# Kernel optimization log

Measured on AMD Instinct MI355X. Metric: run time of the kernel, lower is better.

Reference implementation:

```python
import jax, jax.numpy as jnp
from jax import lax
import numpy as np


def _gru_cell(x, h, wih, whh, bih, bhh):
    # torch.nn.GRUCell math: gates split order (r, z, n)
    gi = x @ wih.T + bih          # (N, 3H)
    gh = h @ whh.T + bhh          # (N, 3H)
    ir, iz, i_n = jnp.split(gi, 3, axis=-1)
    hr, hz, h_n = jnp.split(gh, 3, axis=-1)
    r = jax.nn.sigmoid(ir + hr)
    z = jax.nn.sigmoid(iz + hz)
    n = jnp.tanh(i_n + r * h_n)
    return (1.0 - z) * n + z * h


def _dilated_gru(x, dilation, wih, whh, bih, bhh):
    # h_i depends on h_{i-dilation} -> `dilation` independent chains,
    # scanned jointly with a carried state of shape (B*dilation, H).
    B, S, I = x.shape
    H = whh.shape[1]
    nc = S // dilation  # assumes S % dilation == 0
    xr = x.reshape(B, nc, dilation, I).transpose(1, 0, 2, 3).reshape(nc, B * dilation, I)

    def step(h, xt):
        hn = _gru_cell(xt, h, wih, whh, bih, bhh)
        return hn, hn

    h0 = jnp.zeros((B * dilation, H), x.dtype)
    _, ys = lax.scan(step, h0, xr)  # (nc, B*dilation, H)
    return ys.reshape(nc, B, dilation, H).transpose(1, 0, 2, 3).reshape(B, S, H)


def _encoder(data, fparams, bparams, dilations):
    outs = []
    x = data
    for p, d in zip(fparams, dilations):
        x = _dilated_gru(x, d, *p)
        outs.append(x[:, -1, :])
    x = data[:, ::-1, :]
    for p, d in zip(bparams, dilations):
        x = _dilated_gru(x, d, *p)
        outs.append(x[:, -1, :])
    return jnp.concatenate(outs, axis=1)  # (B, 2*sum(hidden_sizes)) = (B, 400)


def setup_inputs() -> dict:
    key = jax.random.key(0)
    ks = jax.random.split(key, 7)
    B, S = 1024, 512
    sizes = [(1, 100), (100, 50), (50, 50)]  # (input_size, hidden_size) per layer

    def cell(k, iS, H):
        k1, k2, k3, k4 = jax.random.split(k, 4)
        s = 1.0 / np.sqrt(H)  # torch GRUCell init: U(-1/sqrt(H), 1/sqrt(H))
        u = lambda kk, shp: jax.random.uniform(kk, shp, jnp.float32, -s, s)
        return u(k1, (3 * H, iS)), u(k2, (3 * H, H)), u(k3, (3 * H,)), u(k4, (3 * H,))

    d = {"data": jax.random.normal(ks[0], (B, S, 1), jnp.float32)}
    for i, nm in enumerate(["f1", "f2", "f3", "b1", "b2", "b3"]):
        iS, H = sizes[i % 3]
        w1, w2, bb1, bb2 = cell(ks[i + 1], iS, H)
        d[nm + "_wih"] = w1
        d[nm + "_whh"] = w2
        d[nm + "_bih"] = bb1
        d[nm + "_bhh"] = bb2
    return d


def reference(data,
              f1_wih, f1_whh, f1_bih, f1_bhh,
              f2_wih, f2_whh, f2_bih, f2_bhh,
              f3_wih, f3_whh, f3_bih, f3_bhh,
              b1_wih, b1_whh, b1_bih, b1_bhh,
              b2_wih, b2_whh, b2_bih, b2_bhh,
              b3_wih, b3_whh, b3_bih, b3_bhh):
    dilations = (1, 4, 16)
    fparams = [(f1_wih, f1_whh, f1_bih, f1_bhh),
               (f2_wih, f2_whh, f2_bih, f2_bhh),
               (f3_wih, f3_whh, f3_bih, f3_bhh)]
    bparams = [(b1_wih, b1_whh, b1_bih, b1_bhh),
               (b2_wih, b2_whh, b2_bih, b2_bhh),
               (b3_wih, b3_whh, b3_bih, b3_bhh)]
    return _encoder(data, fparams, bparams, dilations)
```

## Files before the change

kernel.cpp:

```cpp
#include <hip/hip_runtime.h>
#include <math.h>

typedef short  s16x8 __attribute__((ext_vector_type(8)));
typedef float  f32x4 __attribute__((ext_vector_type(4)));

static __device__ __forceinline__ float sigf(float x){ return 1.0f/(1.0f+__expf(-x)); }
static __device__ __forceinline__ float tanhf_fast(float x){
  float ax=fabsf(x); float e=__expf(-2.0f*ax); float t=(1.0f-e)/(1.0f+e); return copysignf(t,x);
}
static __device__ __forceinline__ unsigned short f2bf(float x){
  unsigned int u = __float_as_uint(x);
  unsigned int r = (u + 0x7FFFu + ((u >> 16) & 1u)) >> 16;
  return (unsigned short)r;
}
static __device__ __forceinline__ float bf2f(unsigned short b){
  return __uint_as_float(((unsigned int)b) << 16);
}
static __device__ __forceinline__ unsigned int cvt_pk_bf16(float a, float b){
  unsigned int r;
  asm("v_cvt_pk_bf16_f32 %0, %1, %2" : "=v"(r) : "v"(a), "v"(b));
  return r;
}
static __device__ __forceinline__ void fast_barrier(){
  asm volatile("s_waitcnt lgkmcnt(0)" ::: "memory");
  __builtin_amdgcn_s_barrier();
}
static __device__ __forceinline__ float qsum(float v){
  v += __int_as_float(__builtin_amdgcn_mov_dpp(__float_as_int(v),0xB1,0xF,0xF,true));
  v += __int_as_float(__builtin_amdgcn_mov_dpp(__float_as_int(v),0x4E,0xF,0xF,true));
  return v;
}
static __device__ __forceinline__ float rsum4(float v){
  return v + __int_as_float(__builtin_amdgcn_ds_swizzle(__float_as_int(v), 0x101F));
}
static __device__ __forceinline__ float sel4(int c, float4 v){
  float r=v.x; r=(c==1)?v.y:r; r=(c==2)?v.z:r; r=(c==3)?v.w:r; return r;
}

static __device__ __forceinline__ void load_afrag(const float* __restrict__ whh,
                                                  int gate, int tile, int l, int kc,
                                                  s16x8& hi, s16x8& lo){
  const int r  = tile*16 + (l & 15);
  const int kb = kc*32 + (l >> 4)*8;
  #pragma unroll
  for (int j = 0; j < 8; ++j){
    const int k = kb + j;
    const float wv = (r < 100 && k < 100) ? whh[(size_t)(gate*100 + r)*100 + k] : 0.0f;
    const unsigned short hb = f2bf(wv);
    hi[j] = (short)hb;
    lo[j] = (short)f2bf(wv - bf2f(hb));
  }
}

__global__ __launch_bounds__(448, 2)
void gru_l1(const float* __restrict__ data,
            const float* __restrict__ wih_f, const float* __restrict__ whh_f,
            const float* __restrict__ bih_f, const float* __restrict__ bhh_f,
            const float* __restrict__ wih_b, const float* __restrict__ whh_b,
            const float* __restrict__ bih_b, const float* __restrict__ bhh_b,
            float* __restrict__ x1f, float* __restrict__ x1b,
            float* __restrict__ out)
{
  const int dir   = (int)(blockIdx.x >> 6);
  const int blk16 = (int)(blockIdx.x & 63);
  const int t     = (int)threadIdx.x;
  const float* __restrict__ wih = dir ? wih_b : wih_f;
  const float* __restrict__ whh = dir ? whh_b : whh_f;
  const float* __restrict__ bih = dir ? bih_b : bih_f;
  const float* __restrict__ bhh = dir ? bhh_b : bhh_f;
  float* __restrict__ x1 = dir ? x1b : x1f;
  const int obase = dir ? 200 : 0;
  const int b0 = blk16 * 16;

  __shared__ __align__(16) unsigned short hBhi[2][16][136];
  __shared__ __align__(16) unsigned short hBlo[2][16][136];
  __shared__ __align__(16) float xs[512][16];

  for (int i = t; i < 8192; i += 448){
    const int c  = i >> 9;
    const int sL = i & 511;
    xs[sL][c] = data[(size_t)(b0 + c)*512 + (size_t)(dir ? (511 - sL) : sL)];
  }
  { unsigned short* ph = (unsigned short*)hBhi;
    unsigned short* pl = (unsigned short*)hBlo;
    for (int i = t; i < 2*16*136; i += 448){ ph[i] = 0; pl[i] = 0; } }

  const int l  = t & 63;
  const int W  = t >> 6;

  s16x8 AH00,AH01,AH02,AH03, AH10,AH11,AH12,AH13, AH20,AH21,AH22,AH23;
  s16x8 AL00,AL01,AL02,AL03, AL10,AL11,AL12,AL13, AL20,AL21,AL22,AL23;
  #define LDA(G,KC) load_afrag(whh, G, W, l, KC, AH##G##KC, AL##G##KC);
  LDA(0,0) LDA(0,1) LDA(0,2) LDA(0,3)
  LDA(1,0) LDA(1,1) LDA(1,2) LDA(1,3)
  LDA(2,0) LDA(2,1) LDA(2,2) LDA(2,3)
  #undef LDA

  const int mg  = (l >> 4) * 4;
  const int u0  = W*16 + mg;
  const bool uvalid = (u0 < 100);
  const int u0c = uvalid ? u0 : 96;
  const int c   = l & 15;
  const f32x4 wxr4 = *(const f32x4*)&wih[u0c];
  const f32x4 wxz4 = *(const f32x4*)&wih[100 + u0c];
  const f32x4 wxn4 = *(const f32x4*)&wih[200 + u0c];
  const f32x4 bcr4 = *(const f32x4*)&bih[u0c]       + *(const f32x4*)&bhh[u0c];
  const f32x4 bcz4 = *(const f32x4*)&bih[100 + u0c] + *(const f32x4*)&bhh[100 + u0c];
  const f32x4 bxn4 = *(const f32x4*)&bih[200 + u0c];
  const f32x4 bhn4 = *(const f32x4*)&bhh[200 + u0c];
  f32x4 hprev = {0.f,0.f,0.f,0.f};

  __syncthreads();

  const int bn = c;
  const int bg = (l >> 4)*8;

  #pragma unroll 1
  for (int s = 0; s < 512; ++s){
    const int cur = s & 1, nxt = cur ^ 1;

    const s16x8 BH0 = *(const s16x8*)&hBhi[cur][bn][ 0 + bg];
    const s16x8 BL0 = *(const s16x8*)&hBlo[cur][bn][ 0 + bg];
    const s16x8 BH1 = *(const s16x8*)&hBhi[cur][bn][32 + bg];
    const s16x8 BL1 = *(const s16x8*)&hBlo[cur][bn][32 + bg];
    const s16x8 BH2 = *(const s16x8*)&hBhi[cur][bn][64 + bg];
    const s16x8 BL2 = *(const s16x8*)&hBlo[cur][bn][64 + bg];
    const s16x8 BH3 = *(const s16x8*)&hBhi[cur][bn][96 + bg];
    const s16x8 BL3 = *(const s16x8*)&hBlo[cur][bn][96 + bg];

    f32x4 Ca0={0.f,0.f,0.f,0.f}, Cb0={0.f,0.f,0.f,0.f};
    f32x4 Ca1={0.f,0.f,0.f,0.f}, Cb1={0.f,0.f,0.f,0.f};
    f32x4 Ca2={0.f,0.f,0.f,0.f}, Cb2={0.f,0.f,0.f,0.f};
    #define MM(ACC,G,KC) \
      ACC = __builtin_amdgcn_mfma_f32_16x16x32_bf16(AL##G##KC, BH##KC, ACC, 0, 0, 0); \
      ACC = __builtin_amdgcn_mfma_f32_16x16x32_bf16(AH##G##KC, BL##KC, ACC, 0, 0, 0); \
      ACC = __builtin_amdgcn_mfma_f32_16x16x32_bf16(AH##G##KC, BH##KC, ACC, 0, 0, 0);
    MM(Ca0,0,0) MM(Ca1,1,0) MM(Ca2,2,0)
    MM(Cb0,0,2) MM(Cb1,1,2) MM(Cb2,2,2)
    MM(Ca0,0,1) MM(Ca1,1,1) MM(Ca2,2,1)
    MM(Cb0,0,3) MM(Cb1,1,3) MM(Cb2,2,3)
    #undef MM
    const f32x4 sr = Ca0 + Cb0;
    const f32x4 sz = Ca1 + Cb1;
    const f32x4 sn = Ca2 + Cb2;

    const float xc = xs[s][c];
    f32x4 hn;
    #define FIN(I) { \
      const float rr = sigf(sr[I] + fmaf(wxr4[I], xc, bcr4[I])); \
      const float zz = sigf(sz[I] + fmaf(wxz4[I], xc, bcz4[I])); \
      const float nn = tanhf_fast(fmaf(wxn4[I], xc, bxn4[I]) + rr*(sn[I] + bhn4[I])); \
      hn[I] = nn + zz*(hprev[I] - nn); }
    FIN(0) FIN(1) FIN(2) FIN(3)
    #undef FIN
    hprev = hn;

    if (uvalid){
      const unsigned int px = cvt_pk_bf16(hn[0], hn[1]);
      const unsigned int py = cvt_pk_bf16(hn[2], hn[3]);
      const float l0 = hn[0] - __uint_as_float(px << 16);
      const float l1 = hn[1] - __uint_as_float(px & 0xFFFF0000u);
      const float l2 = hn[2] - __uint_as_float(py << 16);
      const float l3 = hn[3] - __uint_as_float(py & 0xFFFF0000u);
      uint2 vhi; vhi.x = px; vhi.y = py;
      uint2 vlo; vlo.x = cvt_pk_bf16(l0, l1); vlo.y = cvt_pk_bf16(l2, l3);
      *(uint2*)&hBhi[nxt][c][u0] = vhi;
      *(uint2*)&hBlo[nxt][c][u0] = vlo;
      if ((s & 3) == 3){
        const int cs = s >> 2;
        const int ch = b0 + c;
        *(f32x4*)&x1[((size_t)cs*1024 + ch)*100 + u0] = hn;
      }
      if (s == 511){
        const int ch = b0 + c;
        *(f32x4*)&out[(size_t)ch*400 + obase + u0] = hn;
      }
    }
    fast_barrier();
  }
}

static __device__ __forceinline__ float l2w(const float* __restrict__ wih,
                                            const float* __restrict__ whh,
                                            int sec, int r, int k){
  if (r >= 50) return 0.f;
  if (sec == 2) return (k < 100) ? wih[(size_t)(100 + r)*100 + k] : 0.f;
  if (sec == 3) return (k >= 104 && k < 154) ? whh[(size_t)(100 + r)*50 + (k - 104)] : 0.f;
  const int ro = (sec == 1) ? 50 : 0;
  if (k < 100) return wih[(size_t)(ro + r)*100 + k];
  if (k >= 104 && k < 154) return whh[(size_t)(ro + r)*50 + (k - 104)];
  return 0.f;
}
static __device__ __forceinline__ void l2_afrag(const float* __restrict__ wih,
                                                const float* __restrict__ whh,
                                                int sec, int tile, int l, int kc,
                                                s16x8& hi, s16x8& lo){
  const int r  = tile*16 + (l & 15);
  const int kb = kc*32 + (l >> 4)*8;
  #pragma unroll
  for (int j = 0; j < 8; ++j){
    const float wv = l2w(wih, whh, sec, r, kb + j);
    const unsigned short hb = f2bf(wv);
    hi[j] = (short)hb;
    lo[j] = (short)f2bf(wv - bf2f(hb));
  }
}

__global__ __launch_bounds__(256, 1)
void gru_l2(const float* __restrict__ x1f, const float* __restrict__ x1b,
            const float* __restrict__ wih_f, const float* __restrict__ whh_f,
            const float* __restrict__ bih_f, const float* __restrict__ bhh_f,
            const float* __restrict__ wih_b, const float* __restrict__ whh_b,
            const float* __restrict__ bih_b, const float* __restrict__ bhh_b,
            float* __restrict__ x2f, float* __restrict__ x2b,
            float* __restrict__ out)
{
  const int dir   = (int)(blockIdx.x >> 6);
  const int blk16 = (int)(blockIdx.x & 63);
  const int t     = (int)threadIdx.x;
  const float* __restrict__ wih = dir ? wih_b : wih_f;
  const float* __restrict__ whh = dir ? whh_b : whh_f;
  const float* __restrict__ bih = dir ? bih_b : bih_f;
  const float* __restrict__ bhh = dir ? bhh_b : bhh_f;
  const float* __restrict__ x1 = dir ? x1b : x1f;
  float* __restrict__ x2 = dir ? x2b : x2f;
  const int obase = dir ? 300 : 100;
  const int b0 = blk16 * 16;

  __shared__ __align__(16) unsigned short hBhi[2][16][168];
  __shared__ __align__(16) unsigned short hBlo[2][16][168];

  { unsigned short* ph = (unsigned short*)hBhi;
    unsigned short* pl = (unsigned short*)hBlo;
    for (int i = t; i < 2*16*168; i += 256){ ph[i] = 0; pl[i] = 0; } }

  const int l = t & 63;
  const int W = t >> 6;

  s16x8 AH00,AH01,AH02,AH03,AH04, AH10,AH11,AH12,AH13,AH14,
        AH20,AH21,AH22,AH23,AH24, AH30,AH31,AH32,AH33,AH34;
  s16x8 AL00,AL01,AL02,AL03,AL04, AL10,AL11,AL12,AL13,AL14,
        AL20,AL21,AL22,AL23,AL24, AL30,AL31,AL32,AL33,AL34;
  #define LDA(SE,KC) l2_afrag(wih, whh, SE, W, l, KC, AH##SE##KC, AL##SE##KC);
  LDA(0,0) LDA(0,1) LDA(0,2) LDA(0,3) LDA(0,4)
  LDA(1,0) LDA(1,1) LDA(1,2) LDA(1,3) LDA(1,4)
  LDA(2,0) LDA(2,1) LDA(2,2) LDA(2,3) LDA(2,4)
  LDA(3,0) LDA(3,1) LDA(3,2) LDA(3,3) LDA(3,4)
  #undef LDA

  const int mg = (l >> 4) * 4;
  const int c  = l & 15;
  const int u0 = W*16 + mg;
  const int ch = b0 + c;
  f32x4 bcr, bcz, bxn, bhn;
  #pragma unroll
  for (int i = 0; i < 4; ++i){
    const int u = (u0 + i < 50) ? (u0 + i) : 49;
    bcr[i] = bih[u]      + bhh[u];
    bcz[i] = bih[50 + u] + bhh[50 + u];
    bxn[i] = bih[100 + u];
    bhn[i] = bhh[100 + u];
  }
  const bool vH = (u0 < 50);
  f32x4 hp = {0.f,0.f,0.f,0.f};

  float* px = x2 + (((size_t)(ch >> 2))*50 + u0)*4 + (ch & 3);
  const size_t X2STRIDE = (size_t)256*50*4;

  const int oct  = t >> 4;
  const int cc   = t & 15;
  const bool stg = (t < 208);
  const int u0x  = oct * 8;

  __syncthreads();

  if (stg){
    const float* p = x1 + ((size_t)0*1024 + (b0 + cc))*100;
    f32x4 va = *(const f32x4*)&p[u0x];
    f32x4 vb = {0.f,0.f,0.f,0.f};
    if (u0x + 4 < 100) vb = *(const f32x4*)&p[u0x + 4];
    unsigned int h0 = cvt_pk_bf16(va[0], va[1]);
    unsigned int h1 = cvt_pk_bf16(va[2], va[3]);
    unsigned int h2 = cvt_pk_bf16(vb[0], vb[1]);
    unsigned int h3 = cvt_pk_bf16(vb[2], vb[3]);
    uint4 vhi; vhi.x=h0; vhi.y=h1; vhi.z=h2; vhi.w=h3;
    uint4 vlo;
    vlo.x = cvt_pk_bf16(va[0]-__uint_as_float(h0<<16), va[1]-__uint_as_float(h0&0xFFFF0000u));
    vlo.y = cvt_pk_bf16(va[2]-__uint_as_float(h1<<16), va[3]-__uint_as_float(h1&0xFFFF0000u));
    vlo.z = cvt_pk_bf16(vb[0]-__uint_as_float(h2<<16), vb[1]-__uint_as_float(h2&0xFFFF0000u));
    vlo.w = cvt_pk_bf16(vb[2]-__uint_as_float(h3<<16), vb[3]-__uint_as_float(h3&0xFFFF0000u));
    *(uint4*)&hBhi[0][cc][u0x] = vhi;
    *(uint4*)&hBlo[0][cc][u0x] = vlo;
  }
  __syncthreads();

  const int bn = c;
  const int bg = (l >> 4)*8;

  #pragma unroll 1
  for (int s = 0; s < 128; ++s){
    const int cur = s & 1, nxt = cur ^ 1;

    f32x4 va = {0.f,0.f,0.f,0.f}, vb = {0.f,0.f,0.f,0.f};
    if (stg){
      const int st = (s + 1 < 128) ? (s + 1) : 127;
      const float* p = x1 + ((size_t)st*1024 + (b0 + cc))*100;
      va = *(const f32x4*)&p[u0x];
      if (u0x + 4 < 100) vb = *(const f32x4*)&p[u0x + 4];
    }

    const s16x8 BH0 = *(const s16x8*)&hBhi[cur][bn][  0 + bg];
    const s16x8 BL0 = *(const s16x8*)&hBlo[cur][bn][  0 + bg];
    const s16x8 BH1 = *(const s16x8*)&hBhi[cur][bn][ 32 + bg];
    const s16x8 BL1 = *(const s16x8*)&hBlo[cur][bn][ 32 + bg];
    const s16x8 BH2 = *(const s16x8*)&hBhi[cur][bn][ 64 + bg];
    const s16x8 BL2 = *(const s16x8*)&hBlo[cur][bn][ 64 + bg];
    const s16x8 BH3 = *(const s16x8*)&hBhi[cur][bn][ 96 + bg];
    const s16x8 BL3 = *(const s16x8*)&hBlo[cur][bn][ 96 + bg];
    const s16x8 BH4 = *(const s16x8*)&hBhi[cur][bn][128 + bg];
    const s16x8 BL4 = *(const s16x8*)&hBlo[cur][bn][128 + bg];

    f32x4 CrA={0.f,0.f,0.f,0.f}, CzA={0.f,0.f,0.f,0.f}, CxA={0.f,0.f,0.f,0.f}, ChA={0.f,0.f,0.f,0.f};
    f32x4 CrB={0.f,0.f,0.f,0.f}, CzB={0.f,0.f,0.f,0.f}, CxB={0.f,0.f,0.f,0.f}, ChB={0.f,0.f,0.f,0.f};
    #define MF(ACC,A,B) ACC = __builtin_amdgcn_mfma_f32_16x16x32_bf16(A, B, ACC, 0, 0, 0);
    #define G4(SET,KC,AOP,BOP) \
      MF(Cr##SET, AOP##0##KC, BOP##KC) MF(Cz##SET, AOP##1##KC, BOP##KC) \
      MF(Cx##SET, AOP##2##KC, BOP##KC) MF(Ch##SET, AOP##3##KC, BOP##KC)
    G4(A,0,AL,BH) G4(B,3,AL,BH) G4(A,1,AL,BH) G4(B,4,AL,BH) G4(A,2,AL,BH)
    G4(A,0,AH,BL) G4(B,3,AH,BL) G4(A,1,AH,BL) G4(B,4,AH,BL) G4(A,2,AH,BL)
    G4(A,0,AH,BH) G4(B,3,AH,BH) G4(A,1,AH,BH) G4(B,4,AH,BH) G4(A,2,AH,BH)
    #undef G4
    #undef MF
    const f32x4 Cr = CrA + CrB;
    const f32x4 Cz = CzA + CzB;
    const f32x4 Cx = CxA + CxB;
    const f32x4 Ch = ChA + ChB;

    f32x4 hn;
    #define FIN(I) { \
      const float rr = sigf(Cr[I] + bcr[I]); \
      const float zz = sigf(Cz[I] + bcz[I]); \
      const float nn = tanhf_fast(Cx[I] + bxn[I] + rr*(Ch[I] + bhn[I])); \
      hn[I] = nn + zz*(hp[I] - nn); }
    FIN(0) FIN(1) FIN(2) FIN(3)
    #undef FIN
    hp = hn;

    if (vH){
      const unsigned int p0 = cvt_pk_bf16(hn[0], hn[1]);
      const unsigned int p1 = cvt_pk_bf16(hn[2], hn[3]);
      const float l0 = hn[0] - __uint_as_float(p0 << 16);
      const float l1 = hn[1] - __uint_as_float(p0 & 0xFFFF0000u);
      const float l2 = hn[2] - __uint_as_float(p1 << 16);
      const float l3 = hn[3] - __uint_as_float(p1 & 0xFFFF0000u);
      uint2 whi; whi.x = p0; whi.y = p1;
      uint2 wlo; wlo.x = cvt_pk_bf16(l0, l1); wlo.y = cvt_pk_bf16(l2, l3);
      *(uint2*)&hBhi[nxt][c][104 + u0] = whi;
      *(uint2*)&hBlo[nxt][c][104 + u0] = wlo;
      if ((s & 3) == 3){
        if (u0 + 0 < 50) px[ 0] = hn[0];
        if (u0 + 1 < 50) px[ 4] = hn[1];
        if (u0 + 2 < 50) px[ 8] = hn[2];
        if (u0 + 3 < 50) px[12] = hn[3];
        px += X2STRIDE;
      }
      if (s == 127){
        if (u0 + 0 < 50) out[(size_t)ch*400 + obase + u0 + 0] = hn[0];
        if (u0 + 1 < 50) out[(size_t)ch*400 + obase + u0 + 1] = hn[1];
        if (u0 + 2 < 50) out[(size_t)ch*400 + obase + u0 + 2] = hn[2];
        if (u0 + 3 < 50) out[(size_t)ch*400 + obase + u0 + 3] = hn[3];
      }
    }

    if (stg){
      unsigned int h0 = cvt_pk_bf16(va[0], va[1]);
      unsigned int h1 = cvt_pk_bf16(va[2], va[3]);
      unsigned int h2 = cvt_pk_bf16(vb[0], vb[1]);
      unsigned int h3 = cvt_pk_bf16(vb[2], vb[3]);
      uint4 vhi; vhi.x=h0; vhi.y=h1; vhi.z=h2; vhi.w=h3;
      uint4 vlo;
      vlo.x = cvt_pk_bf16(va[0]-__uint_as_float(h0<<16), va[1]-__uint_as_float(h0&0xFFFF0000u));
      vlo.y = cvt_pk_bf16(va[2]-__uint_as_float(h1<<16), va[3]-__uint_as_float(h1&0xFFFF0000u));
      vlo.z = cvt_pk_bf16(vb[0]-__uint_as_float(h2<<16), vb[1]-__uint_as_float(h2&0xFFFF0000u));
      vlo.w = cvt_pk_bf16(vb[2]-__uint_as_float(h3<<16), vb[3]-__uint_as_float(h3&0xFFFF0000u));
      *(uint4*)&hBhi[nxt][cc][u0x] = vhi;
      *(uint4*)&hBlo[nxt][cc][u0x] = vlo;
    }
    fast_barrier();
  }
}

__global__ __launch_bounds__(512, 4)
void gru_l3(const float* __restrict__ x2f, const float* __restrict__ x2b,
            const float* __restrict__ wih_f, const float* __restrict__ whh_f,
            const float* __restrict__ bih_f, const float* __restrict__ bhh_f,
            const float* __restrict__ wih_b, const float* __restrict__ whh_b,
            const float* __restrict__ bih_b, const float* __restrict__ bhh_b,
            float* __restrict__ out)
{
  const int dir = (int)(blockIdx.x >> 8);
  const int blk = (int)(blockIdx.x & 255);
  const int t   = (int)threadIdx.x;
  const float* __restrict__ wih = dir ? wih_b : wih_f;
  const float* __restrict__ whh = dir ? whh_b : whh_f;
  const float* __restrict__ bih = dir ? bih_b : bih_f;
  const float* __restrict__ bhh = dir ? bhh_b : bhh_f;
  const float* __restrict__ x2 = dir ? x2b : x2f;
  const int obase = dir ? 350 : 150;
  const int b0 = blk * 4;

  __shared__ __align__(16) float xh[2][104][4];

  const int oct = t >> 3;
  const int u   = (oct > 49) ? 49 : oct;
  const int l   = t & 7;
  const int cb  = 13 * l;
  float4 W0,W1,W2,W3,W4,W5,W6,W7,W8,W9,W10,W11,W12;
  #define L3LW(J, V) { const int g = cb + (J); \
    const float wr_ = (g<50) ? wih[(size_t)(u     )*50+g] : ((g<100)? whh[(size_t)(u     )*50+g-50] : 0.f); \
    const float wz_ = (g<50) ? wih[(size_t)(u + 50)*50+g] : ((g<100)? whh[(size_t)(u + 50)*50+g-50] : 0.f); \
    const float wx_ = (g<50) ? wih[(size_t)(u +100)*50+g] : 0.f; \
    const float wh_ = (g>=50 && g<100) ? whh[(size_t)(u +100)*50+g-50] : 0.f; \
    V = make_float4(wr_, wz_, wx_, wh_); }
  L3LW(0,W0) L3LW(1,W1) L3LW(2,W2) L3LW(3,W3) L3LW(4,W4) L3LW(5,W5) L3LW(6,W6)
  L3LW(7,W7) L3LW(8,W8) L3LW(9,W9) L3LW(10,W10) L3LW(11,W11) L3LW(12,W12)
  #undef L3LW
  const float bcr = bih[u] + bhh[u];
  const float bcz = bih[u+50] + bhh[u+50];
  const float bxn = bih[u+100];
  const float bhn = bhh[u+100];

  for (int i = t; i < 108; i += 512){
    const int bi = (i >= 54) ? 1 : 0;
    const int row = 50 + (i - bi*54);
    *(float4*)&xh[bi][row][0] = make_float4(0.f,0.f,0.f,0.f);
  }
  if (t < 50)
    *(float4*)&xh[0][t][0] = *(const float4*)(x2 + (((size_t)0*256 + blk)*50 + t)*4);
  __syncthreads();

  #pragma unroll 1
  for (int s = 0; s < 32; ++s){
    const int cur = s & 1, nxt = cur ^ 1;
    if (t < 400){
      const float* hb = &xh[cur][cb][0];
      float ar0=0,ar1=0,ar2=0,ar3=0, az0=0,az1=0,az2=0,az3=0;
      float ax0=0,ax1=0,ax2=0,ax3=0, ah0=0,ah1=0,ah2=0,ah3=0;
      #define L3C(J, WV) { const float4 h4 = *(const float4*)(hb + 4*(J)); \
        ar0=fmaf(WV.x,h4.x,ar0); ar1=fmaf(WV.x,h4.y,ar1); ar2=fmaf(WV.x,h4.z,ar2); ar3=fmaf(WV.x,h4.w,ar3); \
        az0=fmaf(WV.y,h4.x,az0); az1=fmaf(WV.y,h4.y,az1); az2=fmaf(WV.y,h4.z,az2); az3=fmaf(WV.y,h4.w,az3); \
        ax0=fmaf(WV.z,h4.x,ax0); ax1=fmaf(WV.z,h4.y,ax1); ax2=fmaf(WV.z,h4.z,ax2); ax3=fmaf(WV.z,h4.w,ax3); \
        ah0=fmaf(WV.w,h4.x,ah0); ah1=fmaf(WV.w,h4.y,ah1); ah2=fmaf(WV.w,h4.z,ah2); ah3=fmaf(WV.w,h4.w,ah3); }
      L3C(0,W0) L3C(1,W1) L3C(2,W2) L3C(3,W3) L3C(4,W4) L3C(5,W5) L3C(6,W6)
      L3C(7,W7) L3C(8,W8) L3C(9,W9) L3C(10,W10) L3C(11,W11) L3C(12,W12)
      #undef L3C
      ar0=qsum(ar0); ar1=qsum(ar1); ar2=qsum(ar2); ar3=qsum(ar3);
      az0=qsum(az0); az1=qsum(az1); az2=qsum(az2); az3=qsum(az3);
      ax0=qsum(ax0); ax1=qsum(ax1); ax2=qsum(ax2); ax3=qsum(ax3);
      ah0=qsum(ah0); ah1=qsum(ah1); ah2=qsum(ah2); ah3=qsum(ah3);
      ar0=rsum4(ar0); ar1=rsum4(ar1); ar2=rsum4(ar2); ar3=rsum4(ar3);
      az0=rsum4(az0); az1=rsum4(az1); az2=rsum4(az2); az3=rsum4(az3);
      ax0=rsum4(ax0); ax1=rsum4(ax1); ax2=rsum4(ax2); ax3=rsum4(ax3);
      ah0=rsum4(ah0); ah1=rsum4(ah1); ah2=rsum4(ah2); ah3=rsum4(ah3);
      if (l < 4){
        const float Ar = sel4(l, make_float4(ar0,ar1,ar2,ar3));
        const float Az = sel4(l, make_float4(az0,az1,az2,az3));
        const float Ax = sel4(l, make_float4(ax0,ax1,ax2,ax3));
        const float Ah = sel4(l, make_float4(ah0,ah1,ah2,ah3));
        const float ho = xh[cur][50+u][l];
        const float r = sigf(Ar + bcr);
        const float z = sigf(Az + bcz);
        const float n = tanhf_fast(Ax + bxn + r*(Ah + bhn));
        const float hnew = n + z*(ho - n);
        xh[nxt][50+u][l] = hnew;
        if (s == 31) out[(size_t)(b0 + l)*400 + obase + u] = hnew;
      }
    } else if (t < 450){
      if (s + 1 < 32){
        const int j = t - 400;
        *(float4*)&xh[nxt][j][0] = *(const float4*)(x2 + (((size_t)(s+1)*256 + blk)*50 + j)*4);
      }
    }
    __syncthreads();
  }
}

extern "C" void kernel_launch(void* const* d_in, const int* in_sizes, int n_in,
                              void* d_out, int out_size, void* d_ws, size_t ws_size,
                              hipStream_t stream)
{
  const float* data   = (const float*)d_in[0];
  const float* f1_wih = (const float*)d_in[1];
  const float* f1_whh = (const float*)d_in[2];
  const float* f1_bih = (const float*)d_in[3];
  const float* f1_bhh = (const float*)d_in[4];
  const float* f2_wih = (const float*)d_in[5];
  const float* f2_whh = (const float*)d_in[6];
  const float* f2_bih = (const float*)d_in[7];
  const float* f2_bhh = (const float*)d_in[8];
  const float* f3_wih = (const float*)d_in[9];
  const float* f3_whh = (const float*)d_in[10];
  const float* f3_bih = (const float*)d_in[11];
  const float* f3_bhh = (const float*)d_in[12];
  const float* b1_wih = (const float*)d_in[13];
  const float* b1_whh = (const float*)d_in[14];
  const float* b1_bih = (const float*)d_in[15];
  const float* b1_bhh = (const float*)d_in[16];
  const float* b2_wih = (const float*)d_in[17];
  const float* b2_whh = (const float*)d_in[18];
  const float* b2_bih = (const float*)d_in[19];
  const float* b2_bhh = (const float*)d_in[20];
  const float* b3_wih = (const float*)d_in[21];
  const float* b3_whh = (const float*)d_in[22];
  const float* b3_bih = (const float*)d_in[23];
  const float* b3_bhh = (const float*)d_in[24];
  float* out = (float*)d_out;

  const size_t X1N = (size_t)128 * 1024 * 100;
  const size_t X2N = (size_t)32 * 256 * 50 * 4;
  if (ws_size < (2 * X1N + 2 * X2N) * sizeof(float)) return;
  float* wsf = (float*)d_ws;
  float* x1f = wsf;
  float* x1b = wsf + X1N;
  float* x2f = wsf + 2 * X1N;
  float* x2b = wsf + 2 * X1N + X2N;

  gru_l1<<<dim3(128), dim3(448), 0, stream>>>(
      data, f1_wih, f1_whh, f1_bih, f1_bhh,
      b1_wih, b1_whh, b1_bih, b1_bhh, x1f, x1b, out);
  gru_l2<<<dim3(128), dim3(256), 0, stream>>>(
      x1f, x1b, f2_wih, f2_whh, f2_bih, f2_bhh,
      b2_wih, b2_whh, b2_bih, b2_bhh, x2f, x2b, out);
  gru_l3<<<dim3(512), dim3(512), 0, stream>>>(
      x2f, x2b, f3_wih, f3_whh, f3_bih, f3_bhh,
      b3_wih, b3_whh, b3_bih, b3_bhh, out);
}
```

Before: 1.027 ms.

## Merge forward and backward directions into one block for layers 1 and 2

Layer 1 and layer 2 kernels now launch half as many blocks, each twice as large, with the forward and backward directions running as two thread groups in the same block and using separate shared-memory state. Layer 1 also drops the shared-memory staging of the input sequence and reads each scalar input straight from global memory every step. The per-step block barrier now synchronizes both directions together, so each direction waits on the slower one. The global input load sits on the critical path of every step, which may add latency to the sequential recurrence.

Result: slower. 3.346 ms (+226.0%).

```diff
diff --git a/kernel.cpp b/kernel.cpp
--- a/kernel.cpp
+++ b/kernel.cpp
@@ -52,7 +52,7 @@
   }
 }
 
-__global__ __launch_bounds__(448, 2)
+__global__ __launch_bounds__(896, 1)
 void gru_l1(const float* __restrict__ data,
             const float* __restrict__ wih_f, const float* __restrict__ whh_f,
             const float* __restrict__ bih_f, const float* __restrict__ bhh_f,
@@ -61,9 +61,11 @@
             float* __restrict__ x1f, float* __restrict__ x1b,
             float* __restrict__ out)
 {
-  const int dir   = (int)(blockIdx.x >> 6);
-  const int blk16 = (int)(blockIdx.x & 63);
+  const int blk16 = (int)blockIdx.x;
   const int t     = (int)threadIdx.x;
+  const int grp   = (t >= 448) ? 1 : 0;
+  const int tt    = t - grp*448;
+  const int dir   = grp;
   const float* __restrict__ wih = dir ? wih_b : wih_f;
   const float* __restrict__ whh = dir ? whh_b : whh_f;
   const float* __restrict__ bih = dir ? bih_b : bih_f;
@@ -72,21 +74,15 @@
   const int obase = dir ? 200 : 0;
   const int b0 = blk16 * 16;
 
-  __shared__ __align__(16) unsigned short hBhi[2][16][136];
-  __shared__ __align__(16) unsigned short hBlo[2][16][136];
-  __shared__ __align__(16) float xs[512][16];
-
-  for (int i = t; i < 8192; i += 448){
-    const int c  = i >> 9;
-    const int sL = i & 511;
-    xs[sL][c] = data[(size_t)(b0 + c)*512 + (size_t)(dir ? (511 - sL) : sL)];
-  }
-  { unsigned short* ph = (unsigned short*)hBhi;
-    unsigned short* pl = (unsigned short*)hBlo;
-    for (int i = t; i < 2*16*136; i += 448){ ph[i] = 0; pl[i] = 0; } }
-
-  const int l  = t & 63;
-  const int W  = t >> 6;
+  __shared__ __align__(16) unsigned short hBhi[2][2][16][136];
+  __shared__ __align__(16) unsigned short hBlo[2][2][16][136];
+
+  { unsigned short* ph = &hBhi[grp][0][0][0];
+    unsigned short* pl = &hBlo[grp][0][0][0];
+    for (int i = tt; i < 2*16*136; i += 448){ ph[i] = 0; pl[i] = 0; } }
+
+  const int l  = tt & 63;
+  const int W  = tt >> 6;
 
   s16x8 AH00,AH01,AH02,AH03, AH10,AH11,AH12,AH13, AH20,AH21,AH22,AH23;
   s16x8 AL00,AL01,AL02,AL03, AL10,AL11,AL12,AL13, AL20,AL21,AL22,AL23;
@@ -110,6 +106,8 @@
   const f32x4 bhn4 = *(const f32x4*)&bhh[200 + u0c];
   f32x4 hprev = {0.f,0.f,0.f,0.f};
 
+  const float* xptr = data + (size_t)(b0 + c)*512;
+
   __syncthreads();
 
   const int bn = c;
@@ -119,14 +117,16 @@
   for (int s = 0; s < 512; ++s){
     const int cur = s & 1, nxt = cur ^ 1;
 
-    const s16x8 BH0 = *(const s16x8*)&hBhi[cur][bn][ 0 + bg];
-    const s16x8 BL0 = *(const s16x8*)&hBlo[cur][bn][ 0 + bg];
-    const s16x8 BH1 = *(const s16x8*)&hBhi[cur][bn][32 + bg];
-    const s16x8 BL1 = *(const s16x8*)&hBlo[cur][bn][32 + bg];
-    const s16x8 BH2 = *(const s16x8*)&hBhi[cur][bn][64 + bg];
-    const s16x8 BL2 = *(const s16x8*)&hBlo[cur][bn][64 + bg];
-    const s16x8 BH3 = *(const s16x8*)&hBhi[cur][bn][96 + bg];
-    const s16x8 BL3 = *(const s16x8*)&hBlo[cur][bn][96 + bg];
+    const float xc = xptr[dir ? (511 - s) : s];
+
+    const s16x8 BH0 = *(const s16x8*)&hBhi[grp][cur][bn][ 0 + bg];
+    const s16x8 BL0 = *(const s16x8*)&hBlo[grp][cur][bn][ 0 + bg];
+    const s16x8 BH1 = *(const s16x8*)&hBhi[grp][cur][bn][32 + bg];
+    const s16x8 BL1 = *(const s16x8*)&hBlo[grp][cur][bn][32 + bg];
+    const s16x8 BH2 = *(const s16x8*)&hBhi[grp][cur][bn][64 + bg];
+    const s16x8 BL2 = *(const s16x8*)&hBlo[grp][cur][bn][64 + bg];
+    const s16x8 BH3 = *(const s16x8*)&hBhi[grp][cur][bn][96 + bg];
+    const s16x8 BL3 = *(const s16x8*)&hBlo[grp][cur][bn][96 + bg];
 
     f32x4 Ca0={0.f,0.f,0.f,0.f}, Cb0={0.f,0.f,0.f,0.f};
     f32x4 Ca1={0.f,0.f,0.f,0.f}, Cb1={0.f,0.f,0.f,0.f};
@@ -144,7 +144,6 @@
     const f32x4 sz = Ca1 + Cb1;
     const f32x4 sn = Ca2 + Cb2;
 
-    const float xc = xs[s][c];
     f32x4 hn;
     #define FIN(I) { \
       const float rr = sigf(sr[I] + fmaf(wxr4[I], xc, bcr4[I])); \
@@ -164,8 +163,8 @@
       const float l3 = hn[3] - __uint_as_float(py & 0xFFFF0000u);
       uint2 vhi; vhi.x = px; vhi.y = py;
       uint2 vlo; vlo.x = cvt_pk_bf16(l0, l1); vlo.y = cvt_pk_bf16(l2, l3);
-      *(uint2*)&hBhi[nxt][c][u0] = vhi;
-      *(uint2*)&hBlo[nxt][c][u0] = vlo;
+      *(uint2*)&hBhi[grp][nxt][c][u0] = vhi;
+      *(uint2*)&hBlo[grp][nxt][c][u0] = vlo;
       if ((s & 3) == 3){
         const int cs = s >> 2;
         const int ch = b0 + c;
@@ -206,7 +205,7 @@
   }
 }
 
-__global__ __launch_bounds__(256, 1)
+__global__ __launch_bounds__(512, 1)
 void gru_l2(const float* __restrict__ x1f, const float* __restrict__ x1b,
             const float* __restrict__ wih_f, const float* __restrict__ whh_f,
             const float* __restrict__ bih_f, const float* __restrict__ bhh_f,
@@ -215,9 +214,11 @@
             float* __restrict__ x2f, float* __restrict__ x2b,
             float* __restrict__ out)
 {
-  const int dir   = (int)(blockIdx.x >> 6);
-  const int blk16 = (int)(blockIdx.x & 63);
+  const int blk16 = (int)blockIdx.x;
   const int t     = (int)threadIdx.x;
+  const int grp   = (t >= 256) ? 1 : 0;
+  const int tt    = t - grp*256;
+  const int dir   = grp;
   const float* __restrict__ wih = dir ? wih_b : wih_f;
   const float* __restrict__ whh = dir ? whh_b : whh_f;
   const float* __restrict__ bih = dir ? bih_b : bih_f;
@@ -227,15 +228,15 @@
   const int obase = dir ? 300 : 100;
   const int b0 = blk16 * 16;
 
-  __shared__ __align__(16) unsigned short hBhi[2][16][168];
-  __shared__ __align__(16) unsigned short hBlo[2][16][168];
-
-  { unsigned short* ph = (unsigned short*)hBhi;
-    unsigned short* pl = (unsigned short*)hBlo;
-    for (int i = t; i < 2*16*168; i += 256){ ph[i] = 0; pl[i] = 0; } }
-
-  const int l = t & 63;
-  const int W = t >> 6;
+  __shared__ __align__(16) unsigned short hBhi[2][2][16][168];
+  __shared__ __align__(16) unsigned short hBlo[2][2][16][168];
+
+  { unsigned short* ph = &hBhi[grp][0][0][0];
+    unsigned short* pl = &hBlo[grp][0][0][0];
+    for (int i = tt; i < 2*16*168; i += 256){ ph[i] = 0; pl[i] = 0; } }
+
+  const int l = tt & 63;
+  const int W = tt >> 6;
 
   s16x8 AH00,AH01,AH02,AH03,AH04, AH10,AH11,AH12,AH13,AH14,
         AH20,AH21,AH22,AH23,AH24, AH30,AH31,AH32,AH33,AH34;
@@ -267,9 +268,9 @@
   float* px = x2 + (((size_t)(ch >> 2))*50 + u0)*4 + (ch & 3);
   const size_t X2STRIDE = (size_t)256*50*4;
 
-  const int oct  = t >> 4;
-  const int cc   = t & 15;
-  const bool stg = (t < 208);
+  const int oct  = tt >> 4;
+  const int cc   = tt & 15;
+  const bool stg = (tt < 208);
   const int u0x  = oct * 8;
 
   __syncthreads();
@@ -289,8 +290,8 @@
     vlo.y = cvt_pk_bf16(va[2]-__uint_as_float(h1<<16), va[3]-__uint_as_float(h1&0xFFFF0000u));
     vlo.z = cvt_pk_bf16(vb[0]-__uint_as_float(h2<<16), vb[1]-__uint_as_float(h2&0xFFFF0000u));
     vlo.w = cvt_pk_bf16(vb[2]-__uint_as_float(h3<<16), vb[3]-__uint_as_float(h3&0xFFFF0000u));
-    *(uint4*)&hBhi[0][cc][u0x] = vhi;
-    *(uint4*)&hBlo[0][cc][u0x] = vlo;
+    *(uint4*)&hBhi[grp][0][cc][u0x] = vhi;
+    *(uint4*)&hBlo[grp][0][cc][u0x] = vlo;
   }
   __syncthreads();
 
@@ -309,16 +310,16 @@
       if (u0x + 4 < 100) vb = *(const f32x4*)&p[u0x + 4];
     }
 
-    const s16x8 BH0 = *(const s16x8*)&hBhi[cur][bn][  0 + bg];
-    const s16x8 BL0 = *(const s16x8*)&hBlo[cur][bn][  0 + bg];
-    const s16x8 BH1 = *(const s16x8*)&hBhi[cur][bn][ 32 + bg];
-    const s16x8 BL1 = *(const s16x8*)&hBlo[cur][bn][ 32 + bg];
-    const s16x8 BH2 = *(const s16x8*)&hBhi[cur][bn][ 64 + bg];
-    const s16x8 BL2 = *(const s16x8*)&hBlo[cur][bn][ 64 + bg];
-    const s16x8 BH3 = *(const s16x8*)&hBhi[cur][bn][ 96 + bg];
-    const s16x8 BL3 = *(const s16x8*)&hBlo[cur][bn][ 96 + bg];
-    const s16x8 BH4 = *(const s16x8*)&hBhi[cur][bn][128 + bg];
-    const s16x8 BL4 = *(const s16x8*)&hBlo[cur][bn][128 + bg];
+    const s16x8 BH0 = *(const s16x8*)&hBhi[grp][cur][bn][  0 + bg];
+    const s16x8 BL0 = *(const s16x8*)&hBlo[grp][cur][bn][  0 + bg];
+    const s16x8 BH1 = *(const s16x8*)&hBhi[grp][cur][bn][ 32 + bg];
+    const s16x8 BL1 = *(const s16x8*)&hBlo[grp][cur][bn][ 32 + bg];
+    const s16x8 BH2 = *(const s16x8*)&hBhi[grp][cur][bn][ 64 + bg];
+    const s16x8 BL2 = *(const s16x8*)&hBlo[grp][cur][bn][ 64 + bg];
+    const s16x8 BH3 = *(const s16x8*)&hBhi[grp][cur][bn][ 96 + bg];
+    const s16x8 BL3 = *(const s16x8*)&hBlo[grp][cur][bn][ 96 + bg];
+    const s16x8 BH4 = *(const s16x8*)&hBhi[grp][cur][bn][128 + bg];
+    const s16x8 BL4 = *(const s16x8*)&hBlo[grp][cur][bn][128 + bg];
 
     f32x4 CrA={0.f,0.f,0.f,0.f}, CzA={0.f,0.f,0.f,0.f}, CxA={0.f,0.f,0.f,0.f}, ChA={0.f,0.f,0.f,0.f};
     f32x4 CrB={0.f,0.f,0.f,0.f}, CzB={0.f,0.f,0.f,0.f}, CxB={0.f,0.f,0.f,0.f}, ChB={0.f,0.f,0.f,0.f};
@@ -355,8 +356,8 @@
       const float l3 = hn[3] - __uint_as_float(p1 & 0xFFFF0000u);
       uint2 whi; whi.x = p0; whi.y = p1;
       uint2 wlo; wlo.x = cvt_pk_bf16(l0, l1); wlo.y = cvt_pk_bf16(l2, l3);
-      *(uint2*)&hBhi[nxt][c][104 + u0] = whi;
-      *(uint2*)&hBlo[nxt][c][104 + u0] = wlo;
+      *(uint2*)&hBhi[grp][nxt][c][104 + u0] = whi;
+      *(uint2*)&hBlo[grp][nxt][c][104 + u0] = wlo;
       if ((s & 3) == 3){
         if (u0 + 0 < 50) px[ 0] = hn[0];
         if (u0 + 1 < 50) px[ 4] = hn[1];
@@ -383,8 +384,8 @@
       vlo.y = cvt_pk_bf16(va[2]-__uint_as_float(h1<<16), va[3]-__uint_as_float(h1&0xFFFF0000u));
       vlo.z = cvt_pk_bf16(vb[0]-__uint_as_float(h2<<16), vb[1]-__uint_as_float(h2&0xFFFF0000u));
       vlo.w = cvt_pk_bf16(vb[2]-__uint_as_float(h3<<16), vb[3]-__uint_as_float(h3&0xFFFF0000u));
-      *(uint4*)&hBhi[nxt][cc][u0x] = vhi;
-      *(uint4*)&hBlo[nxt][cc][u0x] = vlo;
+      *(uint4*)&hBhi[grp][nxt][cc][u0x] = vhi;
+      *(uint4*)&hBlo[grp][nxt][cc][u0x] = vlo;
     }
     fast_barrier();
   }
@@ -525,10 +526,10 @@
   float* x2f = wsf + 2 * X1N;
   float* x2b = wsf + 2 * X1N + X2N;
 
-  gru_l1<<<dim3(128), dim3(448), 0, stream>>>(
+  gru_l1<<<dim3(64), dim3(896), 0, stream>>>(
       data, f1_wih, f1_whh, f1_bih, f1_bhh,
       b1_wih, b1_whh, b1_bih, b1_bhh, x1f, x1b, out);
-  gru_l2<<<dim3(128), dim3(256), 0, stream>>>(
+  gru_l2<<<dim3(64), dim3(512), 0, stream>>>(
       x1f, x1b, f2_wih, f2_whh, f2_bih, f2_bhh,
       b2_wih, b2_whh, b2_bih, b2_bhh, x2f, x2b, out);
   gru_l3<<<dim3(512), dim3(512), 0, stream>>>(
```

## Pack both GRU layer-1 directions into one block with two tiles per wave

Applied to the files above, without the earlier changes.

Layer 1 now launches 64 blocks of 512 threads, where each half of the block handles one direction (forward or backward) for the same 16 batch rows. Each wave computes two 16-row output tiles instead of one, so 4 waves per direction replace 7. The shared x staging buffer is removed, and x is read straight from global memory every step. The aim is fewer waves taking part in each step's barrier and more MFMA work per wave between barriers. The costs are higher register pressure from holding twice the A fragments, a global load on the serial critical path each step, and half as many blocks spread across the CUs.

Result: slower. 2.992 ms (+191.5%).

```diff
diff --git a/kernel.cpp b/kernel.cpp
--- a/kernel.cpp
+++ b/kernel.cpp
@@ -52,7 +52,7 @@
   }
 }
 
-__global__ __launch_bounds__(448, 2)
+__global__ __launch_bounds__(512, 2)
 void gru_l1(const float* __restrict__ data,
             const float* __restrict__ wih_f, const float* __restrict__ whh_f,
             const float* __restrict__ bih_f, const float* __restrict__ bhh_f,
@@ -61,9 +61,11 @@
             float* __restrict__ x1f, float* __restrict__ x1b,
             float* __restrict__ out)
 {
-  const int dir   = (int)(blockIdx.x >> 6);
-  const int blk16 = (int)(blockIdx.x & 63);
+  const int blk16 = (int)blockIdx.x;
   const int t     = (int)threadIdx.x;
+  const int grp   = (t >= 256) ? 1 : 0;
+  const int tt    = t - grp*256;
+  const int dir   = grp;
   const float* __restrict__ wih = dir ? wih_b : wih_f;
   const float* __restrict__ whh = dir ? whh_b : whh_f;
   const float* __restrict__ bih = dir ? bih_b : bih_f;
@@ -72,43 +74,57 @@
   const int obase = dir ? 200 : 0;
   const int b0 = blk16 * 16;
 
-  __shared__ __align__(16) unsigned short hBhi[2][16][136];
-  __shared__ __align__(16) unsigned short hBlo[2][16][136];
-  __shared__ __align__(16) float xs[512][16];
-
-  for (int i = t; i < 8192; i += 448){
-    const int c  = i >> 9;
-    const int sL = i & 511;
-    xs[sL][c] = data[(size_t)(b0 + c)*512 + (size_t)(dir ? (511 - sL) : sL)];
-  }
-  { unsigned short* ph = (unsigned short*)hBhi;
-    unsigned short* pl = (unsigned short*)hBlo;
-    for (int i = t; i < 2*16*136; i += 448){ ph[i] = 0; pl[i] = 0; } }
-
-  const int l  = t & 63;
-  const int W  = t >> 6;
-
-  s16x8 AH00,AH01,AH02,AH03, AH10,AH11,AH12,AH13, AH20,AH21,AH22,AH23;
-  s16x8 AL00,AL01,AL02,AL03, AL10,AL11,AL12,AL13, AL20,AL21,AL22,AL23;
-  #define LDA(G,KC) load_afrag(whh, G, W, l, KC, AH##G##KC, AL##G##KC);
-  LDA(0,0) LDA(0,1) LDA(0,2) LDA(0,3)
-  LDA(1,0) LDA(1,1) LDA(1,2) LDA(1,3)
-  LDA(2,0) LDA(2,1) LDA(2,2) LDA(2,3)
+  __shared__ __align__(16) unsigned short hBhi[2][2][16][136];
+  __shared__ __align__(16) unsigned short hBlo[2][2][16][136];
+
+  { unsigned short* ph = &hBhi[grp][0][0][0];
+    unsigned short* pl = &hBlo[grp][0][0][0];
+    for (int i = tt; i < 2*16*136; i += 256){ ph[i] = 0; pl[i] = 0; } }
+
+  const int l  = tt & 63;
+  const int W  = tt >> 6;
+  const int tA = 2*W, tB = 2*W + 1;
+
+  #define DECLA(G,T) s16x8 AH##G##T##0, AH##G##T##1, AH##G##T##2, AH##G##T##3, \
+                           AL##G##T##0, AL##G##T##1, AL##G##T##2, AL##G##T##3;
+  DECLA(0,a) DECLA(1,a) DECLA(2,a) DECLA(0,b) DECLA(1,b) DECLA(2,b)
+  #undef DECLA
+  #define LDA(G,T,TI) \
+    load_afrag(whh, G, TI, l, 0, AH##G##T##0, AL##G##T##0); \
+    load_afrag(whh, G, TI, l, 1, AH##G##T##1, AL##G##T##1); \
+    load_afrag(whh, G, TI, l, 2, AH##G##T##2, AL##G##T##2); \
+    load_afrag(whh, G, TI, l, 3, AH##G##T##3, AL##G##T##3);
+  LDA(0,a,tA) LDA(1,a,tA) LDA(2,a,tA)
+  LDA(0,b,tB) LDA(1,b,tB) LDA(2,b,tB)
   #undef LDA
 
   const int mg  = (l >> 4) * 4;
-  const int u0  = W*16 + mg;
-  const bool uvalid = (u0 < 100);
-  const int u0c = uvalid ? u0 : 96;
   const int c   = l & 15;
-  const f32x4 wxr4 = *(const f32x4*)&wih[u0c];
-  const f32x4 wxz4 = *(const f32x4*)&wih[100 + u0c];
-  const f32x4 wxn4 = *(const f32x4*)&wih[200 + u0c];
-  const f32x4 bcr4 = *(const f32x4*)&bih[u0c]       + *(const f32x4*)&bhh[u0c];
-  const f32x4 bcz4 = *(const f32x4*)&bih[100 + u0c] + *(const f32x4*)&bhh[100 + u0c];
-  const f32x4 bxn4 = *(const f32x4*)&bih[200 + u0c];
-  const f32x4 bhn4 = *(const f32x4*)&bhh[200 + u0c];
-  f32x4 hprev = {0.f,0.f,0.f,0.f};
+  const int uA0 = tA*16 + mg;
+  const int uB0 = tB*16 + mg;
+  const bool vA = (uA0 < 100);
+  const bool vB = (uB0 < 100);
+  const int uA = vA ? uA0 : 96;
+  const int uB = vB ? uB0 : 96;
+  const f32x4 wxrA = *(const f32x4*)&wih[uA];
+  const f32x4 wxzA = *(const f32x4*)&wih[100 + uA];
+  const f32x4 wxnA = *(const f32x4*)&wih[200 + uA];
+  const f32x4 bcrA = *(const f32x4*)&bih[uA]       + *(const f32x4*)&bhh[uA];
+  const f32x4 bczA = *(const f32x4*)&bih[100 + uA] + *(const f32x4*)&bhh[100 + uA];
+  const f32x4 bxnA = *(const f32x4*)&bih[200 + uA];
+  const f32x4 bhnA = *(const f32x4*)&bhh[200 + uA];
+  const f32x4 wxrB = *(const f32x4*)&wih[uB];
+  const f32x4 wxzB = *(const f32x4*)&wih[100 + uB];
+  const f32x4 wxnB = *(const f32x4*)&wih[200 + uB];
+  const f32x4 bcrB = *(const f32x4*)&bih[uB]       + *(const f32x4*)&bhh[uB];
+  const f32x4 bczB = *(const f32x4*)&bih[100 + uB] + *(const f32x4*)&bhh[100 + uB];
+  const f32x4 bxnB = *(const f32x4*)&bih[200 + uB];
+  const f32x4 bhnB = *(const f32x4*)&bhh[200 + uB];
+  f32x4 hpA = {0.f,0.f,0.f,0.f};
+  f32x4 hpB = {0.f,0.f,0.f,0.f};
+
+  const int ch = b0 + c;
+  const float* xptr = data + (size_t)ch*512;
 
   __syncthreads();
 
@@ -119,62 +135,82 @@
   for (int s = 0; s < 512; ++s){
     const int cur = s & 1, nxt = cur ^ 1;
 
-    const s16x8 BH0 = *(const s16x8*)&hBhi[cur][bn][ 0 + bg];
-    const s16x8 BL0 = *(const s16x8*)&hBlo[cur][bn][ 0 + bg];
-    const s16x8 BH1 = *(const s16x8*)&hBhi[cur][bn][32 + bg];
-    const s16x8 BL1 = *(const s16x8*)&hBlo[cur][bn][32 + bg];
-    const s16x8 BH2 = *(const s16x8*)&hBhi[cur][bn][64 + bg];
-    const s16x8 BL2 = *(const s16x8*)&hBlo[cur][bn][64 + bg];
-    const s16x8 BH3 = *(const s16x8*)&hBhi[cur][bn][96 + bg];
-    const s16x8 BL3 = *(const s16x8*)&hBlo[cur][bn][96 + bg];
-
-    f32x4 Ca0={0.f,0.f,0.f,0.f}, Cb0={0.f,0.f,0.f,0.f};
-    f32x4 Ca1={0.f,0.f,0.f,0.f}, Cb1={0.f,0.f,0.f,0.f};
-    f32x4 Ca2={0.f,0.f,0.f,0.f}, Cb2={0.f,0.f,0.f,0.f};
-    #define MM(ACC,G,KC) \
-      ACC = __builtin_amdgcn_mfma_f32_16x16x32_bf16(AL##G##KC, BH##KC, ACC, 0, 0, 0); \
-      ACC = __builtin_amdgcn_mfma_f32_16x16x32_bf16(AH##G##KC, BL##KC, ACC, 0, 0, 0); \
-      ACC = __builtin_amdgcn_mfma_f32_16x16x32_bf16(AH##G##KC, BH##KC, ACC, 0, 0, 0);
-    MM(Ca0,0,0) MM(Ca1,1,0) MM(Ca2,2,0)
-    MM(Cb0,0,2) MM(Cb1,1,2) MM(Cb2,2,2)
-    MM(Ca0,0,1) MM(Ca1,1,1) MM(Ca2,2,1)
-    MM(Cb0,0,3) MM(Cb1,1,3) MM(Cb2,2,3)
-    #undef MM
-    const f32x4 sr = Ca0 + Cb0;
-    const f32x4 sz = Ca1 + Cb1;
-    const f32x4 sn = Ca2 + Cb2;
-
-    const float xc = xs[s][c];
-    f32x4 hn;
-    #define FIN(I) { \
-      const float rr = sigf(sr[I] + fmaf(wxr4[I], xc, bcr4[I])); \
-      const float zz = sigf(sz[I] + fmaf(wxz4[I], xc, bcz4[I])); \
-      const float nn = tanhf_fast(fmaf(wxn4[I], xc, bxn4[I]) + rr*(sn[I] + bhn4[I])); \
-      hn[I] = nn + zz*(hprev[I] - nn); }
-    FIN(0) FIN(1) FIN(2) FIN(3)
+    const float xc = xptr[dir ? (511 - s) : s];
+
+    const s16x8 BH0 = *(const s16x8*)&hBhi[grp][cur][bn][ 0 + bg];
+    const s16x8 BL0 = *(const s16x8*)&hBlo[grp][cur][bn][ 0 + bg];
+    const s16x8 BH1 = *(const s16x8*)&hBhi[grp][cur][bn][32 + bg];
+    const s16x8 BL1 = *(const s16x8*)&hBlo[grp][cur][bn][32 + bg];
+    const s16x8 BH2 = *(const s16x8*)&hBhi[grp][cur][bn][64 + bg];
+    const s16x8 BL2 = *(const s16x8*)&hBlo[grp][cur][bn][64 + bg];
+    const s16x8 BH3 = *(const s16x8*)&hBhi[grp][cur][bn][96 + bg];
+    const s16x8 BL3 = *(const s16x8*)&hBlo[grp][cur][bn][96 + bg];
+
+    f32x4 C0a={0.f,0.f,0.f,0.f}, C1a={0.f,0.f,0.f,0.f}, C2a={0.f,0.f,0.f,0.f};
+    f32x4 C0b={0.f,0.f,0.f,0.f}, C1b={0.f,0.f,0.f,0.f}, C2b={0.f,0.f,0.f,0.f};
+    #define MF(ACC,A,B) ACC = __builtin_amdgcn_mfma_f32_16x16x32_bf16(A, B, ACC, 0, 0, 0);
+    #define MMKC(KC) \
+      MF(C0a, AL0a##KC, BH##KC) MF(C1a, AL1a##KC, BH##KC) MF(C2a, AL2a##KC, BH##KC) \
+      MF(C0b, AL0b##KC, BH##KC) MF(C1b, AL1b##KC, BH##KC) MF(C2b, AL2b##KC, BH##KC) \
+      MF(C0a, AH0a##KC, BL##KC) MF(C1a, AH1a##KC, BL##KC) MF(C2a, AH2a##KC, BL##KC) \
+      MF(C0b, AH0b##KC, BL##KC) MF(C1b, AH1b##KC, BL##KC) MF(C2b, AH2b##KC, BL##KC) \
+      MF(C0a, AH0a##KC, BH##KC) MF(C1a, AH1a##KC, BH##KC) MF(C2a, AH2a##KC, BH##KC) \
+      MF(C0b, AH0b##KC, BH##KC) MF(C1b, AH1b##KC, BH##KC) MF(C2b, AH2b##KC, BH##KC)
+    MMKC(0) MMKC(1) MMKC(2) MMKC(3)
+    #undef MMKC
+    #undef MF
+
+    f32x4 hnA, hnB;
+    #define FIN(I,SR,SZ,SN,WXR,WXZ,WXN,BCR,BCZ,BXN,BHN,HP,HN) { \
+      const float rr = sigf(SR[I] + fmaf(WXR[I], xc, BCR[I])); \
+      const float zz = sigf(SZ[I] + fmaf(WXZ[I], xc, BCZ[I])); \
+      const float nn = tanhf_fast(fmaf(WXN[I], xc, BXN[I]) + rr*(SN[I] + BHN[I])); \
+      HN[I] = nn + zz*(HP[I] - nn); }
+    FIN(0,C0a,C1a,C2a,wxrA,wxzA,wxnA,bcrA,bczA,bxnA,bhnA,hpA,hnA)
+    FIN(1,C0a,C1a,C2a,wxrA,wxzA,wxnA,bcrA,bczA,bxnA,bhnA,hpA,hnA)
+    FIN(2,C0a,C1a,C2a,wxrA,wxzA,wxnA,bcrA,bczA,bxnA,bhnA,hpA,hnA)
+    FIN(3,C0a,C1a,C2a,wxrA,wxzA,wxnA,bcrA,bczA,bxnA,bhnA,hpA,hnA)
+    FIN(0,C0b,C1b,C2b,wxrB,wxzB,wxnB,bcrB,bczB,bxnB,bhnB,hpB,hnB)
+    FIN(1,C0b,C1b,C2b,wxrB,wxzB,wxnB,bcrB,bczB,bxnB,bhnB,hpB,hnB)
+    FIN(2,C0b,C1b,C2b,wxrB,wxzB,wxnB,bcrB,bczB,bxnB,bhnB,hpB,hnB)
+    FIN(3,C0b,C1b,C2b,wxrB,wxzB,wxnB,bcrB,bczB,bxnB,bhnB,hpB,hnB)
     #undef FIN
-    hprev = hn;
-
-    if (uvalid){
-      const unsigned int px = cvt_pk_bf16(hn[0], hn[1]);
-      const unsigned int py = cvt_pk_bf16(hn[2], hn[3]);
-      const float l0 = hn[0] - __uint_as_float(px << 16);
-      const float l1 = hn[1] - __uint_as_float(px & 0xFFFF0000u);
-      const float l2 = hn[2] - __uint_as_float(py << 16);
-      const float l3 = hn[3] - __uint_as_float(py & 0xFFFF0000u);
+    hpA = hnA; hpB = hnB;
+
+    if (vA){
+      const unsigned int px = cvt_pk_bf16(hnA[0], hnA[1]);
+      const unsigned int py = cvt_pk_bf16(hnA[2], hnA[3]);
+      const float l0 = hnA[0] - __uint_as_float(px << 16);
+      const float l1 = hnA[1] - __uint_as_float(px & 0xFFFF0000u);
+      const float l2 = hnA[2] - __uint_as_float(py << 16);
+      const float l3 = hnA[3] - __uint_as_float(py & 0xFFFF0000u);
       uint2 vhi; vhi.x = px; vhi.y = py;
       uint2 vlo; vlo.x = cvt_pk_bf16(l0, l1); vlo.y = cvt_pk_bf16(l2, l3);
-      *(uint2*)&hBhi[nxt][c][u0] = vhi;
-      *(uint2*)&hBlo[nxt][c][u0] = vlo;
-      if ((s & 3) == 3){
-        const int cs = s >> 2;
-        const int ch = b0 + c;
-        *(f32x4*)&x1[((size_t)cs*1024 + ch)*100 + u0] = hn;
-      }
-      if (s == 511){
-        const int ch = b0 + c;
-        *(f32x4*)&out[(size_t)ch*400 + obase + u0] = hn;
-      }
+      *(uint2*)&hBhi[grp][nxt][c][uA0] = vhi;
+      *(uint2*)&hBlo[grp][nxt][c][uA0] = vlo;
+    }
+    if (vB){
+      const unsigned int px = cvt_pk_bf16(hnB[0], hnB[1]);
+      const unsigned int py = cvt_pk_bf16(hnB[2], hnB[3]);
+      const float l0 = hnB[0] - __uint_as_float(px << 16);
+      const float l1 = hnB[1] - __uint_as_float(px & 0xFFFF0000u);
+      const float l2 = hnB[2] - __uint_as_float(py << 16);
+      const float l3 = hnB[3] - __uint_as_float(py & 0xFFFF0000u);
+      uint2 vhi; vhi.x = px; vhi.y = py;
+      uint2 vlo; vlo.x = cvt_pk_bf16(l0, l1); vlo.y = cvt_pk_bf16(l2, l3);
+      *(uint2*)&hBhi[grp][nxt][c][uB0] = vhi;
+      *(uint2*)&hBlo[grp][nxt][c][uB0] = vlo;
+    }
+
+    if ((s & 3) == 3){
+      const int cs = s >> 2;
+      float* px1 = &x1[((size_t)cs*1024 + ch)*100];
+      if (vA) *(f32x4*)&px1[uA0] = hnA;
+      if (vB) *(f32x4*)&px1[uB0] = hnB;
+    }
+    if (s == 511){
+      if (vA) *(f32x4*)&out[(size_t)ch*400 + obase + uA0] = hnA;
+      if (vB) *(f32x4*)&out[(size_t)ch*400 + obase + uB0] = hnB;
     }
     fast_barrier();
   }
@@ -525,7 +561,7 @@
   float* x2f = wsf + 2 * X1N;
   float* x2b = wsf + 2 * X1N + X2N;
 
-  gru_l1<<<dim3(128), dim3(448), 0, stream>>>(
+  gru_l1<<<dim3(64), dim3(512), 0, stream>>>(
       data, f1_wih, f1_whh, f1_bih, f1_bhh,
       b1_wih, b1_whh, b1_bih, b1_bhh, x1f, x1b, out);
   gru_l2<<<dim3(128), dim3(256), 0, stream>>>(
```
